# Optimization experiments

Measured on AMD Instinct MI355X. Metric: run time of the kernel, lower is better.

The kernel has to match this reference:

```python
import jax, jax.numpy as jnp
import numpy as np
import math

B, S_TOK = 2, 2046
NC = 2
S = S_TOK + NC                 # 2048 total sequence after prepending condition tokens
D, D_INNER, V = 512, 2048, 512
L, H, MAX_SEQ = 6, 8, 2048
DH = D // H
PAD = 0


def setup_inputs() -> dict:
    key = jax.random.key(0)
    ks = iter(jax.random.split(key, 48))
    def nrm(shape, scale=0.02):
        return jax.random.normal(next(ks), shape, jnp.float32) * scale
    inp = {}
    inp["x_tokens"] = jax.random.randint(next(ks), (B, S_TOK), 0, V)
    inp["conditions"] = jax.random.normal(next(ks), (B, NC), jnp.float32)
    inp["times_to_chord"] = jax.random.uniform(next(ks), (B, S_TOK), jnp.float32) * 8.0
    inp["emb"] = nrm((V, D), 0.1).at[PAD].set(0.0)  # padding_idx row zeroed
    inp["pos"] = nrm((1, MAX_SEQ, D), 0.1)
    inp["cond_W1"] = nrm((NC, 1, D // 2)); inp["cond_b1"] = jnp.zeros((NC, D // 2))
    inp["cond_W2"] = nrm((NC, D // 2, D)); inp["cond_b2"] = jnp.zeros((NC, D))
    inp["null_cond"] = nrm((NC, D), 0.1)
    inp["ttc_W"] = nrm((1, D_INNER)); inp["ttc_b"] = jnp.zeros((D_INNER,))
    for nm in ["Wq", "Wk", "Wv", "Wo"]:
        inp[nm] = nrm((L, D, D))
    for nm in ["bq", "bk", "bv", "bo"]:
        inp[nm] = jnp.zeros((L, D))
    inp["E"] = nrm((L, MAX_SEQ, DH), 1.0)  # torch.randn relative-position embedding
    inp["ffn_W1"] = nrm((L, D, D_INNER)); inp["ffn_b1"] = jnp.zeros((L, D_INNER))
    inp["ffn_W2"] = nrm((L, D_INNER, D)); inp["ffn_b2"] = jnp.zeros((L, D))
    inp["ln1_g"] = jnp.ones((L, D)); inp["ln1_b"] = jnp.zeros((L, D))
    inp["ln2_g"] = jnp.ones((L, D)); inp["ln2_b"] = jnp.zeros((L, D))
    inp["fc_W"] = nrm((D, V), 0.1); inp["fc_b"] = jnp.zeros((V,))
    return inp


def _layer_norm(x, g, b, eps=1e-6):
    mu = x.mean(-1, keepdims=True)
    var = ((x - mu) ** 2).mean(-1, keepdims=True)
    return (x - mu) / jnp.sqrt(var + eps) * g + b


def _rel_attn(x, bias, Wq, bq, Wk, bk, Wv, bv, Wo, bo, E):
    # RelativeGlobalAttention: QE masking + skewing trick (Huang et al. 2018)
    Bb, Sq, _ = x.shape
    q = (x @ Wq + bq).reshape(Bb, Sq, H, DH).transpose(0, 2, 1, 3)  # [B,H,S,dh]
    k = (x @ Wk + bk).reshape(Bb, Sq, H, DH).transpose(0, 2, 1, 3)
    v = (x @ Wv + bv).reshape(Bb, Sq, H, DH).transpose(0, 2, 1, 3)
    e = E[MAX_SEQ - Sq:]                                  # [M,dh], M == Sq here
    QE = jnp.einsum('bhld,md->bhlm', q, e)                # [B,H,S,M]
    M = QE.shape[-1]
    # row l keeps columns m >= M-1-l  (torch _qe_masking)
    qe_mask = (jnp.arange(M)[None, :] >= (M - 1 - jnp.arange(Sq))[:, None])
    QE = QE * qe_mask.astype(QE.dtype)
    # skewing: pad one column on the left, reshape, drop first row
    padded = jnp.pad(QE, ((0, 0), (0, 0), (0, 0), (1, 0)))
    Srel = padded.reshape(Bb, H, M + 1, Sq)[:, :, 1:, :]  # [B,H,S,S]
    logits = (jnp.einsum('bhld,bhmd->bhlm', q, k) + Srel) / math.sqrt(DH) + bias
    attn = jax.nn.softmax(logits, axis=-1)
    out = jnp.einsum('bhlm,bhmd->bhld', attn, v)
    out = out.transpose(0, 2, 1, 3).reshape(Bb, Sq, D)
    return out @ Wo + bo


def _forward(x_tokens, conditions, times_to_chord, emb, pos, cond_W1, cond_b1,
             cond_W2, cond_b2, null_cond, ttc_W, ttc_b, Wq, bq, Wk, bk, Wv, bv,
             Wo, bo, E, ffn_W1, ffn_b1, ffn_W2, ffn_b2, ln1_g, ln1_b, ln2_g,
             ln2_b, fc_W, fc_b):
    x = emb[x_tokens] * math.sqrt(D)                      # [B,S_tok,D]
    # generate_mask on tokens padded with -1 for the NC condition slots
    tok_pad = jnp.pad(x_tokens, ((0, 0), (NC, 0)), constant_values=-1)
    causal = jnp.triu(jnp.ones((S, S), bool), 1)          # True above diagonal
    key_pad = tok_pad == PAD                              # [B,S] pad keys
    attn_bias = jnp.where(causal[None] | key_pad[:, None, :],
                          -jnp.inf, 0.0)[:, None]         # [B,1,S,S]
    # condition MLPs with NaN -> learned null-condition substitution
    c = conditions[..., None]                             # [B,NC,1]
    nan = jnp.isnan(c)
    cm = jnp.where(nan, 0.0, c)
    h1 = jax.nn.relu(jnp.einsum('bci,cio->bco', cm, cond_W1) + cond_b1[None])
    ce = jnp.einsum('bci,cio->bco', h1, cond_W2) + cond_b2[None]   # [B,NC,D]
    ce = jnp.where(nan, null_cond[None], ce)
    x = jnp.concatenate([ce, x], axis=1)                  # [B,S,D]
    ttc = jnp.concatenate([jnp.repeat(times_to_chord[:, :1], NC, axis=1),
                           times_to_chord], axis=1)       # [B,S]
    chord = (8.0 - ttc)[..., None] @ ttc_W + ttc_b        # [B,S,D_INNER]
    x = x + pos[:, :S]
    for l in range(L):
        attn_out = _rel_attn(x, attn_bias, Wq[l], bq[l], Wk[l], bk[l],
                             Wv[l], bv[l], Wo[l], bo[l], E[l])
        out1 = _layer_norm(attn_out + x, ln1_g[l], ln1_b[l])
        ffn = jax.nn.relu(out1 @ ffn_W1[l] + ffn_b1[l]) + chord
        ffn = ffn @ ffn_W2[l] + ffn_b2[l]
        x = _layer_norm(out1 + ffn, ln2_g[l], ln2_b[l])
    return x @ fc_W + fc_b                                # [B,S,V]


def reference(x_tokens, conditions, times_to_chord, emb, pos, cond_W1, cond_b1,
              cond_W2, cond_b2, null_cond, ttc_W, ttc_b, Wq, bq, Wk, bk, Wv, bv,
              Wo, bo, E, ffn_W1, ffn_b1, ffn_W2, ffn_b2, ln1_g, ln1_b, ln2_g,
              ln2_b, fc_W, fc_b):
    return _forward(x_tokens, conditions, times_to_chord, emb, pos, cond_W1,
                    cond_b1, cond_W2, cond_b2, null_cond, ttc_W, ttc_b, Wq, bq,
                    Wk, bk, Wv, bv, Wo, bo, E, ffn_W1, ffn_b1, ffn_W2, ffn_b2,
                    ln1_g, ln1_b, ln2_g, ln2_b, fc_W, fc_b)
```

## Files before the change

### kernel.cpp

```cpp
#include <hip/hip_runtime.h>
#include <hip/hip_bf16.h>
#include <math.h>

#define BATCH  2
#define S_TOK  2046
#define NCOND  2
#define SEQ    2048
#define DMODEL 512
#define DINNER 2048
#define NHEAD  8
#define DHEAD  64
#define NLAYER 6
#define VOCAB  512
#define MROWS  (BATCH*SEQ)

#define NSLOT_G 144
#define NSLOTS  (16 * NSLOT_G)

typedef unsigned short bf16u;
typedef __attribute__((ext_vector_type(8))) short s8frag;
typedef __attribute__((ext_vector_type(4))) float f4frag;

__device__ __forceinline__ float b2f(bf16u u) {
  union { unsigned int i; float f; } v; v.i = ((unsigned int)u) << 16; return v.f;
}
__device__ __forceinline__ bf16u f2b(float f) {
  union { float f; unsigned int i; } v; v.f = f;
  unsigned int x = v.i;
  return (bf16u)((x + 0x7fffu + ((x >> 16) & 1u)) >> 16);
}
__device__ __forceinline__ unsigned int pack2(float a, float b) {
  return (unsigned int)f2b(a) | ((unsigned int)f2b(b) << 16);
}

__device__ __forceinline__ void gld16(const bf16u* g, bf16u* l) {
  __builtin_amdgcn_global_load_lds(
      (const __attribute__((address_space(1))) unsigned int*)g,
      (__attribute__((address_space(3))) unsigned int*)l,
      16, 0, 0);
}

#define DPP_ROR(dst, src, N)                                              \
  dst = __int_as_float(__builtin_amdgcn_update_dpp(                       \
      0, __float_as_int(src), 0x120 + (N), 0xF, 0xF, true))

__device__ __forceinline__ int slot_off(int it) {
  int a = it >> 2, b = it & 3;
  return it + 2 * a * (a - 1) + a * b;
}

__global__ __launch_bounds__(256) void wt_all_kernel(
    const float* __restrict__ Wq, const float* __restrict__ Wk,
    const float* __restrict__ Wv, const float* __restrict__ Wo,
    const float* __restrict__ W1, const float* __restrict__ W2,
    const float* __restrict__ fcW,
    bf16u* __restrict__ qkvT, bf16u* __restrict__ oT,
    bf16u* __restrict__ w1T, bf16u* __restrict__ w2T, bf16u* __restrict__ fcT)
{
  int bid = blockIdx.x;
  const float* src; bf16u* dst; int N, K, kt, nt;
  if (bid < 6 * 768) {
    int L = bid / 768, t = bid - L * 768;
    if (t < 256) {
      int mat = t >> 6, tt = t & 63;
      const float* s4[4] = {Wq, Wk, Wv, Wo};
      src = s4[mat] + (size_t)L * DMODEL * DMODEL;
      dst = (mat < 3) ? (qkvT + (size_t)L * 786432 + (size_t)mat * 262144)
                      : (oT + (size_t)L * 262144);
      K = DMODEL; N = DMODEL; kt = tt >> 3; nt = tt & 7;
    } else if (t < 512) {
      int tt = t - 256;
      src = W1 + (size_t)L * DMODEL * DINNER; dst = w1T + (size_t)L * 1048576;
      K = DMODEL; N = DINNER; kt = tt >> 5; nt = tt & 31;
    } else {
      int tt = t - 512;
      src = W2 + (size_t)L * DINNER * DMODEL; dst = w2T + (size_t)L * 1048576;
      K = DINNER; N = DMODEL; kt = tt >> 3; nt = tt & 7;
    }
  } else {
    int tt = bid - 6 * 768;
    src = fcW; dst = fcT;
    K = DMODEL; N = VOCAB; kt = tt >> 3; nt = tt & 7;
  }
  __shared__ bf16u Ls[64][66];
  int tid = threadIdx.x;
  int c = tid & 63, r4 = tid >> 6;
#pragma unroll
  for (int i = 0; i < 16; i++) {
    int r = i * 4 + r4;
    Ls[r][c] = f2b(src[(size_t)(kt * 64 + r) * N + nt * 64 + c]);
  }
  __syncthreads();
#pragma unroll
  for (int i = 0; i < 16; i++) {
    int rr = i * 4 + r4;
    dst[(size_t)(nt * 64 + rr) * K + kt * 64 + c] = Ls[c][rr];
  }
}

__global__ __launch_bounds__(256) void vt_kernel(
    const bf16u* __restrict__ vb, bf16u* __restrict__ vbt)
{
  int bid = blockIdx.x;
  int b = bid >> 8, t = bid & 255;
  int it = t >> 3, h = t & 7;
  __shared__ bf16u Ls[64][66];
  int tid = threadIdx.x;
  int c = tid & 63, r4 = tid >> 6;
#pragma unroll
  for (int i = 0; i < 16; i++) {
    int r = i * 4 + r4;
    Ls[r][c] = vb[(size_t)(b * SEQ + it * 64 + r) * DMODEL + h * DHEAD + c];
  }
  __syncthreads();
#pragma unroll
  for (int i = 0; i < 16; i++) {
    int rr = i * 4 + r4;
    vbt[(size_t)((b * 8 + h) * DHEAD + rr) * SEQ + it * 64 + c] = Ls[c][rr];
  }
}

template <int RB>
__global__ __launch_bounds__(256) void mgemm(
    const bf16u* __restrict__ A, const bf16u* __restrict__ Wt,
    const float* __restrict__ b0, const float* __restrict__ b1,
    const float* __restrict__ b2, const bf16u* __restrict__ Rb,
    float* __restrict__ Cf, bf16u* __restrict__ Cb,
    int M, int N, int K, int mode,
    const float* __restrict__ ttc, const float* __restrict__ ttcW,
    const float* __restrict__ ttcb)
{
  __shared__ bf16u Ab[RB * 32][32];
  __shared__ bf16u Bb[128][32];
  const int tid = threadIdx.x;
  const int lane = tid & 63, wave = tid >> 6;
  const int quad = lane >> 4, l16 = lane & 15;
  const int wm = wave >> 1, wn = wave & 1;

  const int nwg = gridDim.x * gridDim.y;
  const int lin = blockIdx.y * gridDim.x + blockIdx.x;
  const int swz = (lin & 7) * (nwg >> 3) + (lin >> 3);
  const int bx = swz % gridDim.x, by = swz / gridDim.x;
  const int row0 = bx * (RB * 32), col0 = by * 128;

  f4frag acc[RB][4];
#pragma unroll
  for (int i = 0; i < RB; i++)
#pragma unroll
    for (int j = 0; j < 4; j++) acc[i][j] = (f4frag){0.f, 0.f, 0.f, 0.f};

  for (int k0 = 0; k0 < K; k0 += 32) {
    if (k0) __syncthreads();
    if constexpr (RB >= 2) {
#pragma unroll
      for (int i = 0; i < RB / 2; i++) {
        int chunk = i * 256 + tid;
        int r = chunk >> 2, q = chunk & 3;
        gld16(&A[(size_t)(row0 + r) * K + k0 + q * 8], &Ab[0][0] + chunk * 8);
      }
    } else {
      if (tid < 128) {
        int r = tid >> 2, q = tid & 3;
        gld16(&A[(size_t)(row0 + r) * K + k0 + q * 8], &Ab[0][0] + tid * 8);
      }
    }
#pragma unroll
    for (int i = 0; i < 2; i++) {
      int chunk = i * 256 + tid;
      int r = chunk >> 2, q = chunk & 3;
      gld16(&Wt[(size_t)(col0 + r) * K + k0 + q * 8], &Bb[0][0] + chunk * 8);
    }
    __syncthreads();
    s8frag af[RB], bfr[4];
#pragma unroll
    for (int t = 0; t < RB; t++)
      af[t] = *(const s8frag*)&Ab[wm * (RB * 16) + t * 16 + l16][quad * 8];
#pragma unroll
    for (int t = 0; t < 4; t++)
      bfr[t] = *(const s8frag*)&Bb[wn * 64 + t * 16 + l16][quad * 8];
#pragma unroll
    for (int mt = 0; mt < RB; mt++)
#pragma unroll
      for (int nt = 0; nt < 4; nt++)
        acc[mt][nt] = __builtin_amdgcn_mfma_f32_16x16x32_bf16(
            af[mt], bfr[nt], acc[mt][nt], 0, 0, 0);
  }

#pragma unroll
  for (int mt = 0; mt < RB; mt++) {
#pragma unroll
    for (int r = 0; r < 4; r++) {
      int m = row0 + wm * (RB * 16) + mt * 16 + quad * 4 + r;
      float tval = 0.f;
      if (mode == 2) {
        int bb = m >> 11, s = m & (SEQ - 1);
        int sp = (s < NCOND) ? 0 : (s - NCOND);
        tval = 8.0f - ttc[bb * S_TOK + sp];
      }
#pragma unroll
      for (int nt = 0; nt < 4; nt++) {
        int n = col0 + wn * 64 + nt * 16 + l16;
        if (mode == 4) {
          int sel = n >> 9, nn = n & 511;
          float bv = (sel == 0) ? b0[nn] : ((sel == 1) ? b1[nn] : b2[nn]);
          Cb[(size_t)sel * MROWS * DMODEL + (size_t)m * DMODEL + nn]
              = f2b(acc[mt][nt][r] + bv);
        } else {
          float v = acc[mt][nt][r] + b0[n];
          if (mode == 1)      v += b2f(Rb[(size_t)m * N + n]);
          else if (mode == 2) v = fmaxf(v, 0.f) + tval * ttcW[n] + ttcb[n];
          if (mode == 3) Cf[(size_t)m * N + n] = v;
          else           Cb[(size_t)m * N + n] = f2b(v);
        }
      }
    }
  }
}

__global__ __launch_bounds__(256) void ln_kernel(
    const bf16u* __restrict__ X, const float* __restrict__ g,
    const float* __restrict__ bta, bf16u* __restrict__ Y)
{
  int row = blockIdx.x, tid = threadIdx.x;
  unsigned int pr = *(const unsigned int*)&X[(size_t)row * DMODEL + 2 * tid];
  float x0 = b2f((bf16u)(pr & 0xffff)), x1 = b2f((bf16u)(pr >> 16));
  __shared__ float red[8];
  int wv = tid >> 6, ln = tid & 63;
  float s = x0 + x1;
  for (int off = 32; off; off >>= 1) s += __shfl_xor(s, off);
  if (ln == 0) red[wv] = s;
  __syncthreads();
  float mu = (red[0] + red[1] + red[2] + red[3]) * (1.0f / DMODEL);
  float d0 = x0 - mu, d1 = x1 - mu;
  float vs = d0 * d0 + d1 * d1;
  for (int off = 32; off; off >>= 1) vs += __shfl_xor(vs, off);
  if (ln == 0) red[4 + wv] = vs;
  __syncthreads();
  float var = (red[4] + red[5] + red[6] + red[7]) * (1.0f / DMODEL);
  float rstd = rsqrtf(var + 1e-6f);
  float y0 = d0 * rstd * g[2 * tid]     + bta[2 * tid];
  float y1 = d1 * rstd * g[2 * tid + 1] + bta[2 * tid + 1];
  *(unsigned int*)&Y[(size_t)row * DMODEL + 2 * tid] = pack2(y0, y1);
}

__global__ __launch_bounds__(256) void tok_embed_kernel(
    const int* __restrict__ toks, const float* __restrict__ emb,
    const float* __restrict__ pos, bf16u* __restrict__ xb)
{
  int sp = blockIdx.x, b = blockIdx.y;
  int s = sp + NCOND;
  int tok = toks[b * S_TOK + sp];
  const float* er = emb + (size_t)tok * DMODEL;
  const float* pr = pos + (size_t)s * DMODEL;
  size_t ro = ((size_t)b * SEQ + s) * DMODEL;
  int d = threadIdx.x * 2;
  float v0 = er[d]     * 22.62741699796952f + pr[d];
  float v1 = er[d + 1] * 22.62741699796952f + pr[d + 1];
  *(unsigned int*)&xb[ro + d] = pack2(v0, v1);
}

__global__ __launch_bounds__(256) void cond_embed_kernel(
    const float* __restrict__ conds, const float* __restrict__ W1,
    const float* __restrict__ b1, const float* __restrict__ W2w,
    const float* __restrict__ b2, const float* __restrict__ nullc,
    const float* __restrict__ pos, bf16u* __restrict__ xb)
{
  int ci = blockIdx.x, b = blockIdx.y, tid = threadIdx.x;
  float c = conds[b * NCOND + ci];
  bool cn = isnan(c);
  float cm = cn ? 0.f : c;
  __shared__ float h1[DMODEL / 2];
  h1[tid] = fmaxf(cm * W1[ci * (DMODEL/2) + tid] + b1[ci * (DMODEL/2) + tid], 0.f);
  __syncthreads();
  for (int d = tid; d < DMODEL; d += 256) {
    float acc = b2[ci * DMODEL + d];
    for (int i = 0; i < DMODEL / 2; i++)
      acc = fmaf(h1[i], W2w[((size_t)ci * (DMODEL/2) + i) * DMODEL + d], acc);
    float ce = cn ? nullc[ci * DMODEL + d] : acc;
    xb[((size_t)b * SEQ + ci) * DMODEL + d] = f2b(ce + pos[(size_t)ci * DMODEL + d]);
  }
}

__global__ __launch_bounds__(256) void e_conv_kernel(
    const float* __restrict__ E, bf16u* __restrict__ Eb)
{
  int i = (blockIdx.x * 256 + threadIdx.x) * 4;
  float4 v = *(const float4*)&E[i];
  ushort4 o;
  o.x = f2b(v.x); o.y = f2b(v.y); o.z = f2b(v.z); o.w = f2b(v.w);
  *(ushort4*)&Eb[i] = o;
}

#define PS_SWZ(row) ((((row) >> 2) & 7) << 3)

__global__ __launch_bounds__(256) void attn_part(
    const bf16u* __restrict__ Q, const bf16u* __restrict__ K,
    const bf16u* __restrict__ Vt_g, const bf16u* __restrict__ Eb16,
    const int* __restrict__ toks, bf16u* __restrict__ pacc,
    float* __restrict__ pstat)
{
  const int d = blockIdx.x;
  const int xcd = d & 7, rank = d >> 3;
  const int g  = xcd * 2 + (rank >> 8);
  const int t  = rank & 255;
  const int it = 31 - (t >> 3);
  const int c  = t & 7;
  if (4 * c > it) return;
  const int slot = g * NSLOT_G + slot_off(it) + c;
  const int b = g >> 3, h = g & 7;
  const int i0 = it * 64;

  __shared__ bf16u Kb[64][72];
  __shared__ bf16u Vt[64][72];
  __shared__ bf16u Ebs[128][72];
  __shared__ float padv[64];
  bf16u (*Ps)[72] = Kb;

  const int tid  = threadIdx.x;
  const int lane = tid & 63;
  const int wave = tid >> 6;
  const int quad = lane >> 4;
  const int l16  = lane & 15;

  const bf16u* qr = Q + ((size_t)(b * SEQ + i0 + wave * 16 + l16)) * DMODEL + h * DHEAD;
  s8frag q0 = *(const s8frag*)&qr[quad * 8];
  s8frag q1 = *(const s8frag*)&qr[32 + quad * 8];

  float m_run[4], l_run[4];
  f4frag acc[4];
#pragma unroll
  for (int r = 0; r < 4; r++) { m_run[r] = -1e30f; l_run[r] = 0.f; }
#pragma unroll
  for (int dt = 0; dt < 4; dt++) acc[dt] = (f4frag){0.f, 0.f, 0.f, 0.f};

  const int js0 = 4 * c;
  const int jsE = min(4 * c + 4, it + 1);
  const size_t vtbase = (size_t)(g * DHEAD) * SEQ;

  for (int js = js0; js < jsE; js++) {
    const int j0 = js * 64;
    const int m0 = 1984 - i0 + j0;
    __syncthreads();

#pragma unroll
    for (int e = 0; e < 2; e++) {
      int cc = e * 256 + tid;
      int jr = cc >> 3, doff = (cc & 7) * 8;
      *(uint4*)&Kb[jr][doff] =
          *(const uint4*)&K[((size_t)(b * SEQ + j0 + jr)) * DMODEL + h * DHEAD + doff];
    }
#pragma unroll
    for (int e = 0; e < 2; e++) {
      int cc = e * 256 + tid;
      int dr = cc >> 3, joff = (cc & 7) * 8;
      *(uint4*)&Vt[dr][joff] =
          *(const uint4*)&Vt_g[vtbase + (size_t)dr * SEQ + j0 + joff];
    }
    if (js == js0) {
#pragma unroll
      for (int e = 0; e < 4; e++) {
        int cc = e * 256 + tid;
        int er = cc >> 3, doff = (cc & 7) * 8;
        int m = m0 + er; int row = m > SEQ - 1 ? SEQ - 1 : m;
        *(uint4*)&Ebs[m & 127][doff] = *(const uint4*)&Eb16[(size_t)row * DHEAD + doff];
      }
    } else {
#pragma unroll
      for (int e = 0; e < 2; e++) {
        int cc = e * 256 + tid;
        int er = 64 + (cc >> 3), doff = (cc & 7) * 8;
        int m = m0 + er; int row = m > SEQ - 1 ? SEQ - 1 : m;
        *(uint4*)&Ebs[m & 127][doff] = *(const uint4*)&Eb16[(size_t)row * DHEAD + doff];
      }
    }
    if (tid < 64) {
      int j = j0 + tid;
      bool pad = (j >= NCOND) && (toks[b * S_TOK + j - NCOND] == 0);
      padv[tid] = pad ? -1e30f : 0.f;
    }
    __syncthreads();

    f4frag sc[4];
#pragma unroll
    for (int nt = 0; nt < 4; nt++) {
      s8frag k0 = *(const s8frag*)&Kb[nt * 16 + l16][quad * 8];
      s8frag k1 = *(const s8frag*)&Kb[nt * 16 + l16][32 + quad * 8];
      f4frag cc = (f4frag){0.f, 0.f, 0.f, 0.f};
      cc = __builtin_amdgcn_mfma_f32_16x16x32_bf16(q0, k0, cc, 0, 0, 0);
      cc = __builtin_amdgcn_mfma_f32_16x16x32_bf16(q1, k1, cc, 0, 0, 0);
      sc[nt] = cc;
    }

    f4frag qef[5];
#pragma unroll
    for (int f = 0; f < 5; f++) {
      int ct = f + 3 - wave;
      int m = m0 + ct * 16 + l16;
      const bf16u* erow = &Ebs[m & 127][0];
      s8frag e0 = *(const s8frag*)&erow[quad * 8];
      s8frag e1 = *(const s8frag*)&erow[32 + quad * 8];
      f4frag cc = (f4frag){0.f, 0.f, 0.f, 0.f};
      cc = __builtin_amdgcn_mfma_f32_16x16x32_bf16(q0, e0, cc, 0, 0, 0);
      cc = __builtin_amdgcn_mfma_f32_16x16x32_bf16(q1, e1, cc, 0, 0, 0);
      qef[f] = cc;
    }

    __syncthreads();

    float pvv[4];
#pragma unroll
    for (int nt = 0; nt < 4; nt++) pvv[nt] = padv[nt * 16 + l16];

    float s[4][4], mx[4];
#pragma unroll
    for (int r = 0; r < 4; r++) {
      int rloc = wave * 16 + quad * 4 + r;
      int ig = i0 + rloc;
      int t2 = quad * 4 + r;
      int v = 63 - 16 * wave + l16 - t2;
      int srcl = (lane & 48) | (v & 15);
      bool hiSrc = (l16 < 15 - t2);
#pragma unroll
      for (int nt = 0; nt < 4; nt++) {
        float pre = hiSrc ? qef[nt + 1][r] : qef[nt][r];
        float qe = __shfl(pre, srcl);
        int jl = nt * 16 + l16;
        float sv = (sc[nt][r] + qe) * 0.125f + pvv[nt];
        if (j0 + jl > ig) sv = -1e30f;
        s[nt][r] = sv;
      }
      float m = fmaxf(fmaxf(s[0][r], s[1][r]), fmaxf(s[2][r], s[3][r]));
      float tr;
      DPP_ROR(tr, m, 1); m = fmaxf(m, tr);
      DPP_ROR(tr, m, 2); m = fmaxf(m, tr);
      DPP_ROR(tr, m, 4); m = fmaxf(m, tr);
      DPP_ROR(tr, m, 8); m = fmaxf(m, tr);
      mx[r] = m;
    }
    float alpha[4];
#pragma unroll
    for (int r = 0; r < 4; r++) {
      float m_new = fmaxf(m_run[r], mx[r]);
      alpha[r] = __expf(m_run[r] - m_new);
      float psum = 0.f;
      int rloc = wave * 16 + quad * 4 + r;
#pragma unroll
      for (int nt = 0; nt < 4; nt++) {
        float p = __expf(s[nt][r] - m_new);
        Ps[rloc][(nt * 16 + l16) ^ PS_SWZ(rloc)] = f2b(p);
        psum += p;
      }
      float tr;
      DPP_ROR(tr, psum, 1); psum += tr;
      DPP_ROR(tr, psum, 2); psum += tr;
      DPP_ROR(tr, psum, 4); psum += tr;
      DPP_ROR(tr, psum, 8); psum += tr;
      l_run[r] = l_run[r] * alpha[r] + psum;
      m_run[r] = m_new;
    }
#pragma unroll
    for (int dt = 0; dt < 4; dt++)
#pragma unroll
      for (int r = 0; r < 4; r++) acc[dt][r] *= alpha[r];

    {
      int prow = wave * 16 + l16;
      int psw = PS_SWZ(prow);
      s8frag p0 = *(const s8frag*)&Ps[prow][(quad * 8) ^ psw];
      s8frag p1 = *(const s8frag*)&Ps[prow][(32 + quad * 8) ^ psw];
#pragma unroll
      for (int dt = 0; dt < 4; dt++) {
        s8frag v0 = *(const s8frag*)&Vt[dt * 16 + l16][quad * 8];
        s8frag v1 = *(const s8frag*)&Vt[dt * 16 + l16][32 + quad * 8];
        acc[dt] = __builtin_amdgcn_mfma_f32_16x16x32_bf16(p0, v0, acc[dt], 0, 0, 0);
        acc[dt] = __builtin_amdgcn_mfma_f32_16x16x32_bf16(p1, v1, acc[dt], 0, 0, 0);
      }
    }
  }

#pragma unroll
  for (int r = 0; r < 4; r++) {
    int rloc = wave * 16 + quad * 4 + r;
    if (l16 == 0) {
      pstat[(size_t)slot * 128 + rloc]      = m_run[r];
      pstat[(size_t)slot * 128 + 64 + rloc] = l_run[r];
    }
#pragma unroll
    for (int dt = 0; dt < 4; dt++)
      pacc[(size_t)slot * 4096 + rloc * 64 + dt * 16 + l16] = f2b(acc[dt][r]);
  }
}

__global__ __launch_bounds__(256) void attn_combine(
    const bf16u* __restrict__ pacc, const float* __restrict__ pstat,
    bf16u* __restrict__ O)
{
  int bid = blockIdx.x;
  int g = bid >> 5, it = bid & 31;
  int b = g >> 3, h = g & 7;
  int i0 = it * 64;
  int nc = (it >> 2) + 1;
  int base = g * NSLOT_G + slot_off(it);
  int tid = threadIdx.x;
  int row = tid >> 2, ql = tid & 3;

  float m_tot = -1e30f;
  float mc[8], lc[8];
#pragma unroll
  for (int c = 0; c < 8; c++) {
    if (c < nc) {
      size_t pb = (size_t)(base + c) * 128;
      mc[c] = pstat[pb + row];
      lc[c] = pstat[pb + 64 + row];
      m_tot = fmaxf(m_tot, mc[c]);
    }
  }
  float l_tot = 0.f, w[8];
#pragma unroll
  for (int c = 0; c < 8; c++) {
    if (c < nc) { w[c] = __expf(mc[c] - m_tot); l_tot += w[c] * lc[c]; }
    else w[c] = 0.f;
  }
  float inv = 1.0f / l_tot;

  float out[16];
#pragma unroll
  for (int k = 0; k < 16; k++) out[k] = 0.f;
#pragma unroll
  for (int c = 0; c < 8; c++) {
    if (c >= nc) break;
    const bf16u* pa = pacc + (size_t)(base + c) * 4096 + row * 64 + ql * 16;
#pragma unroll
    for (int k = 0; k < 16; k++) out[k] += w[c] * b2f(pa[k]);
  }
  bf16u* ob = O + ((size_t)(b * SEQ + i0 + row)) * DMODEL + h * DHEAD + ql * 16;
#pragma unroll
  for (int k = 0; k < 16; k++) ob[k] = f2b(out[k] * inv);
}

extern "C" void kernel_launch(void* const* d_in, const int* in_sizes, int n_in,
                              void* d_out, int out_size, void* d_ws, size_t ws_size,
                              hipStream_t stream) {
  const int*   toks  = (const int*)  d_in[0];
  const float* conds = (const float*)d_in[1];
  const float* ttc   = (const float*)d_in[2];
  const float* emb   = (const float*)d_in[3];
  const float* pos   = (const float*)d_in[4];
  const float* cW1   = (const float*)d_in[5];
  const float* cb1   = (const float*)d_in[6];
  const float* cW2   = (const float*)d_in[7];
  const float* cb2   = (const float*)d_in[8];
  const float* nullc = (const float*)d_in[9];
  const float* ttcW  = (const float*)d_in[10];
  const float* ttcb  = (const float*)d_in[11];
  const float* Wq    = (const float*)d_in[12];
  const float* Wk    = (const float*)d_in[13];
  const float* Wv    = (const float*)d_in[14];
  const float* Wo    = (const float*)d_in[15];
  const float* bq    = (const float*)d_in[16];
  const float* bk    = (const float*)d_in[17];
  const float* bv    = (const float*)d_in[18];
  const float* bo    = (const float*)d_in[19];
  const float* E     = (const float*)d_in[20];
  const float* fW1   = (const float*)d_in[21];
  const float* fb1   = (const float*)d_in[22];
  const float* fW2   = (const float*)d_in[23];
  const float* fb2   = (const float*)d_in[24];
  const float* ln1g  = (const float*)d_in[25];
  const float* ln1b  = (const float*)d_in[26];
  const float* ln2g  = (const float*)d_in[27];
  const float* ln2b  = (const float*)d_in[28];
  const float* fcW   = (const float*)d_in[29];
  const float* fcb   = (const float*)d_in[30];

  const size_t MB1 = 1024 * 1024;
  const size_t MD = (size_t)MROWS * DMODEL;
  char* p = (char*)d_ws;
  bf16u* xb    = (bf16u*)p; p += 4 * MB1;
  bf16u* qkvb  = (bf16u*)p; p += 12 * MB1;
  bf16u* hidb  = (bf16u*)p; p += 16 * MB1;
  float* pstat_old = (float*)p; p += 1 * MB1;
  bf16u* vbt   = (bf16u*)p; p += 4 * MB1;
  bf16u* ebf   = (bf16u*)p; p += 1536 * 1024;
  bf16u* WqkvT = (bf16u*)p; p += 9 * MB1;
  bf16u* WoT   = (bf16u*)p; p += 3 * MB1;
  bf16u* W1T   = (bf16u*)p; p += 12 * MB1;
  bf16u* W2T   = (bf16u*)p; p += 12 * MB1;
  bf16u* fcT   = (bf16u*)p; p += 512 * 1024;
  (void)pstat_old;
  bf16u* qb = qkvb;
  bf16u* kb = qkvb + MD;
  bf16u* vb = qkvb + 2 * MD;
  bf16u* out1b = kb;
  bf16u* t1b   = vb;
  bf16u* pacc  = vb;
  float* pstat = (float*)(pacc + (size_t)NSLOTS * 4096);

  cond_embed_kernel<<<dim3(NCOND, BATCH), 256, 0, stream>>>(
      conds, cW1, cb1, cW2, cb2, nullc, pos, xb);
  tok_embed_kernel<<<dim3(S_TOK, BATCH), 256, 0, stream>>>(toks, emb, pos, xb);
  wt_all_kernel<<<6 * 768 + 64, 256, 0, stream>>>(Wq, Wk, Wv, Wo, fW1, fW2, fcW,
      WqkvT, WoT, W1T, W2T, fcT);
  e_conv_kernel<<<(NLAYER * SEQ * DHEAD) / 1024, 256, 0, stream>>>(E, ebf);

  dim3 gQKV(MROWS / 128, 1536 / 128);
  dim3 gFF1(MROWS / 128, DINNER / 128);
  dim3 gN512(MROWS / 32, DMODEL / 128);

  for (int l = 0; l < NLAYER; l++) {
    mgemm<4><<<gQKV, 256, 0, stream>>>(xb, WqkvT + (size_t)l * 786432,
        bq + l * DMODEL, bk + l * DMODEL, bv + l * DMODEL, nullptr,
        nullptr, qkvb, MROWS, 1536, DMODEL, 4, nullptr, nullptr, nullptr);

    vt_kernel<<<512, 256, 0, stream>>>(vb, vbt);
    attn_part<<<4096, 256, 0, stream>>>(qb, kb, vbt,
        ebf + (size_t)l * SEQ * DHEAD, toks, pacc, pstat);
    attn_combine<<<512, 256, 0, stream>>>(pacc, pstat, qb);

    mgemm<1><<<gN512, 256, 0, stream>>>(qb, WoT + (size_t)l * 262144,
        bo + l * DMODEL, nullptr, nullptr, xb,
        nullptr, t1b, MROWS, DMODEL, DMODEL, 1, nullptr, nullptr, nullptr);
    ln_kernel<<<MROWS, 256, 0, stream>>>(t1b, ln1g + l * DMODEL, ln1b + l * DMODEL,
        out1b);

    mgemm<4><<<gFF1, 256, 0, stream>>>(out1b, W1T + (size_t)l * 1048576,
        fb1 + l * DINNER, nullptr, nullptr, nullptr,
        nullptr, hidb, MROWS, DINNER, DMODEL, 2, ttc, ttcW, ttcb);
    mgemm<1><<<gN512, 256, 0, stream>>>(hidb, W2T + (size_t)l * 1048576,
        fb2 + l * DMODEL, nullptr, nullptr, out1b,
        nullptr, t1b, MROWS, DMODEL, DINNER, 1, nullptr, nullptr, nullptr);
    ln_kernel<<<MROWS, 256, 0, stream>>>(t1b, ln2g + l * DMODEL, ln2b + l * DMODEL,
        xb);
  }

  mgemm<1><<<gN512, 256, 0, stream>>>(xb, fcT,
      fcb, nullptr, nullptr, nullptr,
      (float*)d_out, nullptr, MROWS, VOCAB, DMODEL, 3, nullptr, nullptr, nullptr);
}
```

Measured before the change: 1.337 ms.

## Double GEMM k-tile to 64 with XOR-swizzled LDS and compact attention grid

The GEMM kernel now stages 64-wide K slices per iteration, halving the barrier and loop count. It also applies an XOR swizzle on 16-byte octets so that LDS fragment reads avoid bank conflicts. The attention partial kernel launch shrinks from 4096 blocks, many of which exited immediately, to exactly NSLOTS blocks, with a small loop that decodes (tile, chunk) per block. The larger tiles double the LDS footprint per workgroup, which may reduce occupancy.

```diff
diff --git a/kernel.cpp b/kernel.cpp
--- a/kernel.cpp
+++ b/kernel.cpp
@@ -130,8 +130,8 @@
     const float* __restrict__ ttc, const float* __restrict__ ttcW,
     const float* __restrict__ ttcb)
 {
-  __shared__ bf16u Ab[RB * 32][32];
-  __shared__ bf16u Bb[128][32];
+  __shared__ bf16u Ab[RB * 32][64];
+  __shared__ bf16u Bb[128][64];
   const int tid = threadIdx.x;
   const int lane = tid & 63, wave = tid >> 6;
   const int quad = lane >> 4, l16 = lane & 15;
@@ -149,41 +149,43 @@
 #pragma unroll
     for (int j = 0; j < 4; j++) acc[i][j] = (f4frag){0.f, 0.f, 0.f, 0.f};
 
-  for (int k0 = 0; k0 < K; k0 += 32) {
+  for (int k0 = 0; k0 < K; k0 += 64) {
     if (k0) __syncthreads();
-    if constexpr (RB >= 2) {
-#pragma unroll
-      for (int i = 0; i < RB / 2; i++) {
-        int chunk = i * 256 + tid;
-        int r = chunk >> 2, q = chunk & 3;
-        gld16(&A[(size_t)(row0 + r) * K + k0 + q * 8], &Ab[0][0] + chunk * 8);
-      }
-    } else {
-      if (tid < 128) {
-        int r = tid >> 2, q = tid & 3;
-        gld16(&A[(size_t)(row0 + r) * K + k0 + q * 8], &Ab[0][0] + tid * 8);
-      }
-    }
-#pragma unroll
-    for (int i = 0; i < 2; i++) {
-      int chunk = i * 256 + tid;
-      int r = chunk >> 2, q = chunk & 3;
-      gld16(&Wt[(size_t)(col0 + r) * K + k0 + q * 8], &Bb[0][0] + chunk * 8);
+#pragma unroll
+    for (int i = 0; i < RB; i++) {
+      int c = i * 256 + tid;
+      int r = c >> 3, goct = (c & 7) ^ (r & 7);
+      gld16(&A[(size_t)(row0 + r) * K + k0 + goct * 8], &Ab[0][0] + c * 8);
+    }
+#pragma unroll
+    for (int i = 0; i < 4; i++) {
+      int c = i * 256 + tid;
+      int r = c >> 3, goct = (c & 7) ^ (r & 7);
+      gld16(&Wt[(size_t)(col0 + r) * K + k0 + goct * 8], &Bb[0][0] + c * 8);
     }
     __syncthreads();
-    s8frag af[RB], bfr[4];
-#pragma unroll
-    for (int t = 0; t < RB; t++)
-      af[t] = *(const s8frag*)&Ab[wm * (RB * 16) + t * 16 + l16][quad * 8];
-#pragma unroll
-    for (int t = 0; t < 4; t++)
-      bfr[t] = *(const s8frag*)&Bb[wn * 64 + t * 16 + l16][quad * 8];
-#pragma unroll
-    for (int mt = 0; mt < RB; mt++)
-#pragma unroll
-      for (int nt = 0; nt < 4; nt++)
-        acc[mt][nt] = __builtin_amdgcn_mfma_f32_16x16x32_bf16(
-            af[mt], bfr[nt], acc[mt][nt], 0, 0, 0);
+#pragma unroll
+    for (int kk = 0; kk < 2; kk++) {
+      s8frag af[RB], bfr[4];
+#pragma unroll
+      for (int t = 0; t < RB; t++) {
+        int ar = wm * (RB * 16) + t * 16 + l16;
+        int aoct = ((kk << 2) | quad) ^ (ar & 7);
+        af[t] = *(const s8frag*)&Ab[ar][aoct * 8];
+      }
+#pragma unroll
+      for (int t = 0; t < 4; t++) {
+        int br = wn * 64 + t * 16 + l16;
+        int boct = ((kk << 2) | quad) ^ (br & 7);
+        bfr[t] = *(const s8frag*)&Bb[br][boct * 8];
+      }
+#pragma unroll
+      for (int mt = 0; mt < RB; mt++)
+#pragma unroll
+        for (int nt = 0; nt < 4; nt++)
+          acc[mt][nt] = __builtin_amdgcn_mfma_f32_16x16x32_bf16(
+              af[mt], bfr[nt], acc[mt][nt], 0, 0, 0);
+    }
   }
 
 #pragma unroll
@@ -301,11 +303,11 @@
 {
   const int d = blockIdx.x;
   const int xcd = d & 7, rank = d >> 3;
-  const int g  = xcd * 2 + (rank >> 8);
-  const int t  = rank & 255;
-  const int it = 31 - (t >> 3);
-  const int c  = t & 7;
-  if (4 * c > it) return;
+  const int g = xcd * 2 + (rank >= NSLOT_G);
+  int rem = (rank >= NSLOT_G) ? rank - NSLOT_G : rank;
+  int it = 31;
+  for (;;) { int ch = (it >> 2) + 1; if (rem < ch) break; rem -= ch; --it; }
+  const int c = rem;
   const int slot = g * NSLOT_G + slot_off(it) + c;
   const int b = g >> 3, h = g & 7;
   const int i0 = it * 64;
@@ -613,7 +615,7 @@
         nullptr, qkvb, MROWS, 1536, DMODEL, 4, nullptr, nullptr, nullptr);
 
     vt_kernel<<<512, 256, 0, stream>>>(vb, vbt);
-    attn_part<<<4096, 256, 0, stream>>>(qb, kb, vbt,
+    attn_part<<<NSLOTS, 256, 0, stream>>>(qb, kb, vbt,
         ebf + (size_t)l * SEQ * DHEAD, toks, pacc, pstat);
     attn_combine<<<512, 256, 0, stream>>>(pacc, pstat, qb);
 
```

Measured after the change: 1.226 ms. 8.3% less time.
